# Kernel optimization log

Hardware: AMD Instinct MI355X
Metric: run time of the kernel (lower is better)

## Reference

```python
import jax, jax.numpy as jnp
import numpy as np

R, S, V, F = 4096, 128, 3, 35  # n_rays, n_samples, n_views(=3 fixed by rgb_fc), in_feat_ch+3


def _kaiming(key, fan_out, fan_in):
    return jax.random.normal(key, (fan_out, fan_in), jnp.float32) * jnp.sqrt(2.0 / fan_in)


def setup_inputs() -> dict:
    key = jax.random.key(0)
    ks = jax.random.split(key, 8)
    rgb_feat = jax.random.normal(ks[0], (R, S, V, F), jnp.float32)
    # base_fc: 105 -> 64 -> 32
    bw1, bw2 = _kaiming(ks[1], 64, 105), _kaiming(ks[2], 32, 64)
    # vis_fc: 32 -> 32 -> 32
    vw1, vw2 = _kaiming(ks[3], 32, 32), _kaiming(ks[4], 32, 32)
    # rgb_fc: 96 -> 32 -> 16 -> 3
    rw1, rw2, rw3 = _kaiming(ks[5], 32, 96), _kaiming(ks[6], 16, 32), _kaiming(ks[7], 3, 16)
    z = jnp.zeros
    return {
        "rgb_feat": rgb_feat,
        "bw1": bw1, "bb1": z((64,)), "bw2": bw2, "bb2": z((32,)),
        "vw1": vw1, "vb1": z((32,)), "vw2": vw2, "vb2": z((32,)),
        "rw1": rw1, "rb1": z((32,)), "rw2": rw2, "rb2": z((16,)), "rw3": rw3, "rb3": z((3,)),
    }


def _lin(x, w, b):
    return x @ w.T + b


def reference(rgb_feat, bw1, bb1, bw2, bb2, vw1, vb1, vw2, vb2,
              rw1, rb1, rw2, rb2, rw3, rb3):
    elu = jax.nn.elu
    num_views = rgb_feat.shape[2]
    rgb_in = rgb_feat[..., :3]
    # fused mean/variance over the views axis (dim=2)
    mean = jnp.mean(rgb_feat, axis=2, keepdims=True)          # [R,S,1,F]
    var = jnp.mean((rgb_feat - mean) ** 2, axis=2, keepdims=True)
    globalfeat = jnp.concatenate([mean, var], axis=-1)         # [R,S,1,2F]
    x = jnp.concatenate(
        [jnp.broadcast_to(globalfeat, (rgb_feat.shape[0], rgb_feat.shape[1], num_views, globalfeat.shape[-1])),
         rgb_feat], axis=-1)                                   # [R,S,V,3F]
    x = elu(_lin(elu(_lin(x, bw1, bb1)), bw2, bb2))            # [R,S,V,32]
    x_vis = elu(_lin(elu(_lin(x / num_views, vw1, vb1)), vw2, vb2))
    x = x + x_vis
    h = x.reshape(x.shape[0], x.shape[1], num_views * 32)      # [R,S,96]
    rgb_out = jax.nn.sigmoid(_lin(elu(_lin(elu(_lin(h, rw1, rb1)), rw2, rb2)), rw3, rb3))
    return (rgb_in, rgb_out)
```

## Files before the change

### kernel.cpp

```cpp
#include <hip/hip_runtime.h>
#include <hip/hip_bf16.h>

#define NPTS      524288
#define OUT2_BASE 4718592
#define NBLK64    8192

using bf16x8 = __attribute__((ext_vector_type(8))) short;
using f32x4  = __attribute__((ext_vector_type(4))) float;

#define MFMA(a, b, c) __builtin_amdgcn_mfma_f32_16x16x32_bf16(a, b, c, 0, 0, 0)


__device__ __forceinline__ ushort f2bf(float f) {
    union { float f; unsigned u; } v; v.f = f;
    unsigned u = v.u;
    unsigned r = u + 0x7fffu + ((u >> 16) & 1u);
    return (ushort)(r >> 16);
}
__device__ __forceinline__ uint pack2(float a, float b) {
    union { __hip_bfloat162 h; uint u; } cv;
    cv.h = __float22bfloat162_rn(make_float2(a, b));
    return cv.u;
}
__device__ __forceinline__ float eluf(float x) {
    return fmaxf(x, 0.f) + __expf(fminf(x, 0.f)) - 1.f;
}
__device__ __forceinline__ float sigm(float x) { return 1.f / (1.f + __expf(-x)); }

__device__ __forceinline__ void load8(const float* __restrict__ p, float* d) {
    __builtin_memcpy(d, p, 16);
    __builtin_memcpy(d + 4, p + 4, 16);
}
__device__ __forceinline__ bf16x8 pk8(const float* x) {
    union { uint4 u; bf16x8 h; } cv;
    cv.u = make_uint4(pack2(x[0], x[1]), pack2(x[2], x[3]),
                      pack2(x[4], x[5]), pack2(x[6], x[7]));
    return cv.h;
}
__device__ __forceinline__ bf16x8 pk4u(uint a, uint b, uint c, uint d) {
    union { uint4 u; bf16x8 h; } cv;
    cv.u = make_uint4(a, b, c, d);
    return cv.h;
}
__device__ __forceinline__ bf16x8 ldw(const ushort* p) { return *(const bf16x8*)p; }

__global__ void prep_k(const float* __restrict__ bw1, const float* __restrict__ bw2,
                       const float* __restrict__ vw1, const float* __restrict__ vw2,
                       const float* __restrict__ rw1, const float* __restrict__ rw2,
                       ushort* __restrict__ w)
{
    int i = blockIdx.x * 256 + threadIdx.x;
    if (i < 6144) {
        int n = i / 96, k = i % 96;
        float val = 0.f;
        if (k < 35)                 val = bw1[n * 105 + k];
        else if (k >= 40 && k < 75) val = bw1[n * 105 + 35 + (k - 40)];
        w[i] = f2bf(val);
    } else if (i < 10752) {
        int t = i - 6144, n = t / 72, k = t % 72;
        w[i] = f2bf(k < 35 ? bw1[n * 105 + 70 + k] : 0.f);
    } else if (i < 13056) {
        int t = i - 10752, n = t / 72, k = t % 72;
        w[i] = f2bf(k < 64 ? bw2[n * 64 + k] : 0.f);
    } else if (i < 14336) {
        int t = i - 13056, n = t / 40, k = t % 40;
        w[i] = f2bf(k < 32 ? vw1[n * 32 + k] * (1.f / 3.f) : 0.f);
    } else if (i < 15616) {
        int t = i - 14336, n = t / 40, k = t % 40;
        w[i] = f2bf(k < 32 ? vw2[n * 32 + k] : 0.f);
    } else if (i < 18944) {
        int t = i - 15616, n = t / 104, k = t % 104;
        w[i] = f2bf(k < 96 ? rw1[n * 96 + k] : 0.f);
    } else if (i < 19584) {
        int t = i - 18944, n = t / 40, k = t % 40;
        w[i] = f2bf(k < 32 ? rw2[n * 32 + k] : 0.f);
    }
}

__global__ __launch_bounds__(256, 4) void mlp_k(
    const float* __restrict__ feat, const ushort* __restrict__ w,
    const float* __restrict__ bb1, const float* __restrict__ bb2,
    const float* __restrict__ vb1, const float* __restrict__ vb2,
    const float* __restrict__ rb1, const float* __restrict__ rb2,
    const float* __restrict__ rw3, const float* __restrict__ rb3,
    float* __restrict__ out)
{
    __shared__ __align__(16) ushort sh[4][4608];

    const int tid  = threadIdx.x;
    const int wave = tid >> 6;
    const int lane = tid & 63;
    const int n16  = lane & 15;
    const int quad = lane >> 4;
    char* const RA = (char*)sh[wave];
    char* const RB = (char*)sh[wave] + 6144;
    const int sw7 = n16 & 7;
    const int sw3 = n16 & 3;

    const long long pbase = (long long)blockIdx.x * 64 + wave * 16;
    const long long pt    = pbase + n16;
    const float* row = feat + pt * 105;

    const ushort* WG = w;
    const ushort* WF = w + 6144;
    const ushort* W2 = w + 10752;
    const ushort* V1 = w + 13056;
    const ushort* V2 = w + 14336;
    const ushort* R1 = w + 15616;
    const ushort* R2 = w + 18944;

    {
        float* o1 = out + pbase * 9;
        const float* f0 = feat + pbase * 105;
#pragma unroll
        for (int t = 0; t < 3; ++t) {
            int i = lane + t * 64;
            if (t < 2 || lane < 16) {
                int p = i / 9, r = i - p * 9, v = r / 3, c = r - v * 3;
                o1[i] = f0[p * 105 + v * 35 + c];
            }
        }
    }

    float A0[8], A1[8], A2[8];
    load8(row + 8 * quad,      A0);
    load8(row + 35 + 8 * quad, A1);
    load8(row + 70 + 8 * quad, A2);
    float E0[8] = {0,0,0,0,0,0,0,0}, E1[8] = {0,0,0,0,0,0,0,0}, E2[8] = {0,0,0,0,0,0,0,0};
    if (quad == 0) {
        load8(row + 32, E0);
        load8(row + 67, E1);
        if (pt == (long long)NPTS - 1) {
            E2[0] = row[102]; E2[1] = row[103]; E2[2] = row[104];
        } else {
            load8(row + 102, E2);
        }
    }
    float M[8], Vv[8], M4[8], V4[8];
#pragma unroll
    for (int j = 0; j < 8; ++j) {
        float a = A0[j], b = A1[j], c = A2[j];
        float m = (a + b + c) * (1.f / 3.f);
        float da = a - m, db = b - m, dc = c - m;
        M[j] = m; Vv[j] = (da * da + db * db + dc * dc) * (1.f / 3.f);
        float a4 = E0[j], b4 = E1[j], c4 = E2[j];
        float m4 = (a4 + b4 + c4) * (1.f / 3.f);
        float e4 = a4 - m4, f4 = b4 - m4, g4 = c4 - m4;
        M4[j] = m4; V4[j] = (e4 * e4 + f4 * f4 + g4 * g4) * (1.f / 3.f);
    }
    uint vPK[4], v4PK[4], m4PK[4];
#pragma unroll
    for (int i = 0; i < 4; ++i) {
        vPK[i]  = pack2(Vv[2 * i], Vv[2 * i + 1]);
        v4PK[i] = pack2(V4[2 * i], V4[2 * i + 1]);
        m4PK[i] = pack2(M4[2 * i], M4[2 * i + 1]);
    }
    bf16x8 XAv[3], XBv[3];
    XAv[0] = pk8(A0); XAv[1] = pk8(A1); XAv[2] = pk8(A2);
    const bf16x8 ZF = pk4u(0u, 0u, 0u, 0u);
    XBv[0] = ZF; XBv[1] = ZF; XBv[2] = ZF;
    if (quad == 0) { XBv[0] = pk8(E0); XBv[1] = pk8(E1); XBv[2] = pk8(E2); }
    const bf16x8 G0 = pk8(M);
    const int prevAddr = ((lane + 48) & 63) * 4;
    uint G1u[4], G2u[4];
#pragma unroll
    for (int i = 0; i < 4; ++i) {
        uint bv  = (uint)__builtin_amdgcn_ds_bpermute(prevAddr, (int)vPK[i]);
        uint bv4 = (uint)__builtin_amdgcn_ds_bpermute(prevAddr, (int)v4PK[i]);
        G1u[i] = (quad == 0) ? m4PK[i] : bv;
        G2u[i] = (quad == 0) ? bv : ((quad == 1) ? bv4 : 0u);
    }
    const bf16x8 G1 = pk4u(G1u[0], G1u[1], G1u[2], G1u[3]);
    const bf16x8 G2 = pk4u(G2u[0], G2u[1], G2u[2], G2u[3]);

    const f32x4 Z = {0.f, 0.f, 0.f, 0.f};

#pragma unroll
    for (int ntl = 0; ntl < 4; ++ntl) {
        const ushort* WGb = WG + (ntl * 16 + n16) * 96 + quad * 8;
        f32x4 Cg = MFMA(ldw(WGb), G0, Z);
        Cg = MFMA(ldw(WGb + 32), G1, Cg);
        Cg = MFMA(ldw(WGb + 64), G2, Cg);
        const ushort* WFb = WF + (ntl * 16 + n16) * 72 + quad * 8;
        const bf16x8 wf0 = ldw(WFb), wf1 = ldw(WFb + 32);
        const float4 bq = *(const float4*)(bb1 + ntl * 16 + quad * 4);
#pragma unroll
        for (int v = 0; v < 3; ++v) {
            f32x4 C = MFMA(wf0, XAv[v], Cg);
            C = MFMA(wf1, XBv[v], C);
            float e0 = eluf(C[0] + bq.x), e1 = eluf(C[1] + bq.y);
            float e2 = eluf(C[2] + bq.z), e3 = eluf(C[3] + bq.w);
            uint2 u; u.x = pack2(e0, e1); u.y = pack2(e2, e3);
            int slot = (ntl * 2 + (quad >> 1)) ^ sw7;
            *(uint2*)(RA + v * 2048 + n16 * 128 + slot * 16 + (quad & 1) * 8) = u;
        }
    }

    float h2r[3][2][4];
#pragma unroll
    for (int v = 0; v < 3; ++v) {
        const bf16x8 ha = *(const bf16x8*)(RA + v * 2048 + n16 * 128 + ((0 + quad) ^ sw7) * 16);
        const bf16x8 hb = *(const bf16x8*)(RA + v * 2048 + n16 * 128 + ((4 + quad) ^ sw7) * 16);
#pragma unroll
        for (int n2 = 0; n2 < 2; ++n2) {
            const ushort* W2b = W2 + (n2 * 16 + n16) * 72 + quad * 8;
            f32x4 C = MFMA(ldw(W2b), ha, Z);
            C = MFMA(ldw(W2b + 32), hb, C);
            const float4 bq = *(const float4*)(bb2 + n2 * 16 + quad * 4);
            float e0 = eluf(C[0] + bq.x), e1 = eluf(C[1] + bq.y);
            float e2 = eluf(C[2] + bq.z), e3 = eluf(C[3] + bq.w);
            h2r[v][n2][0] = e0; h2r[v][n2][1] = e1;
            h2r[v][n2][2] = e2; h2r[v][n2][3] = e3;
            uint2 u; u.x = pack2(e0, e1); u.y = pack2(e2, e3);
            int slot = (n2 * 2 + (quad >> 1)) ^ sw3;
            *(uint2*)(RB + v * 1024 + n16 * 64 + slot * 16 + (quad & 1) * 8) = u;
        }
    }

#pragma unroll
    for (int v = 0; v < 3; ++v) {
        const bf16x8 hf = *(const bf16x8*)(RB + v * 1024 + n16 * 64 + ((quad ^ sw3) * 16));
#pragma unroll
        for (int n2 = 0; n2 < 2; ++n2) {
            f32x4 C = MFMA(ldw(V1 + (n2 * 16 + n16) * 40 + quad * 8), hf, Z);
            const float4 bq = *(const float4*)(vb1 + n2 * 16 + quad * 4);
            float e0 = eluf(C[0] + bq.x), e1 = eluf(C[1] + bq.y);
            float e2 = eluf(C[2] + bq.z), e3 = eluf(C[3] + bq.w);
            uint2 u; u.x = pack2(e0, e1); u.y = pack2(e2, e3);
            int slot = (n2 * 2 + (quad >> 1)) ^ sw3;
            *(uint2*)(RA + v * 1024 + n16 * 64 + slot * 16 + (quad & 1) * 8) = u;
        }
    }

#pragma unroll
    for (int v = 0; v < 3; ++v) {
        const bf16x8 tf = *(const bf16x8*)(RA + v * 1024 + n16 * 64 + ((quad ^ sw3) * 16));
#pragma unroll
        for (int n2 = 0; n2 < 2; ++n2) {
            f32x4 C = MFMA(ldw(V2 + (n2 * 16 + n16) * 40 + quad * 8), tf, Z);
            const float4 bq = *(const float4*)(vb2 + n2 * 16 + quad * 4);
            float x0 = h2r[v][n2][0] + eluf(C[0] + bq.x);
            float x1 = h2r[v][n2][1] + eluf(C[1] + bq.y);
            float x2v = h2r[v][n2][2] + eluf(C[2] + bq.z);
            float x3 = h2r[v][n2][3] + eluf(C[3] + bq.w);
            uint2 u; u.x = pack2(x0, x1); u.y = pack2(x2v, x3);
            int slot = (4 * v + 2 * n2 + (quad >> 1)) ^ sw3;
            *(uint2*)(RB + n16 * 192 + slot * 16 + (quad & 1) * 8) = u;
        }
    }

    f32x4 CR[2] = {Z, Z};
#pragma unroll
    for (int v = 0; v < 3; ++v) {
        const bf16x8 xf = *(const bf16x8*)(RB + n16 * 192 + (((4 * v + quad) ^ sw3) * 16));
#pragma unroll
        for (int n2 = 0; n2 < 2; ++n2)
            CR[n2] = MFMA(ldw(R1 + (n2 * 16 + n16) * 104 + v * 32 + quad * 8), xf, CR[n2]);
    }
#pragma unroll
    for (int n2 = 0; n2 < 2; ++n2) {
        const float4 bq = *(const float4*)(rb1 + n2 * 16 + quad * 4);
        float e0 = eluf(CR[n2][0] + bq.x), e1 = eluf(CR[n2][1] + bq.y);
        float e2 = eluf(CR[n2][2] + bq.z), e3 = eluf(CR[n2][3] + bq.w);
        uint2 u; u.x = pack2(e0, e1); u.y = pack2(e2, e3);
        int slot = (n2 * 2 + (quad >> 1)) ^ sw3;
        *(uint2*)(RA + n16 * 64 + slot * 16 + (quad & 1) * 8) = u;
    }

    const bf16x8 rf = *(const bf16x8*)(RA + n16 * 64 + ((quad ^ sw3) * 16));
    f32x4 C3 = MFMA(ldw(R2 + n16 * 40 + quad * 8), rf, Z);
    const float4 bq2 = *(const float4*)(rb2 + quad * 4);
    float r0 = eluf(C3[0] + bq2.x), r1v = eluf(C3[1] + bq2.y);
    float r2v = eluf(C3[2] + bq2.z), r3 = eluf(C3[3] + bq2.w);

    const float4 w30 = *(const float4*)(rw3 + 0 * 16 + quad * 4);
    const float4 w31 = *(const float4*)(rw3 + 1 * 16 + quad * 4);
    const float4 w32 = *(const float4*)(rw3 + 2 * 16 + quad * 4);
    float s0 = r0 * w30.x + r1v * w30.y + r2v * w30.z + r3 * w30.w;
    float s1 = r0 * w31.x + r1v * w31.y + r2v * w31.z + r3 * w31.w;
    float s2 = r0 * w32.x + r1v * w32.y + r2v * w32.z + r3 * w32.w;
    s0 += __shfl_xor(s0, 16); s0 += __shfl_xor(s0, 32);
    s1 += __shfl_xor(s1, 16); s1 += __shfl_xor(s1, 32);
    s2 += __shfl_xor(s2, 16); s2 += __shfl_xor(s2, 32);
    if (quad == 0) {
        float* o2 = out + OUT2_BASE + pt * 3;
        o2[0] = sigm(s0 + rb3[0]);
        o2[1] = sigm(s1 + rb3[1]);
        o2[2] = sigm(s2 + rb3[2]);
    }
}

extern "C" void kernel_launch(void* const* d_in, const int* in_sizes, int n_in,
                              void* d_out, int out_size, void* d_ws, size_t ws_size,
                              hipStream_t stream) {
    const float* feat = (const float*)d_in[0];
    const float* bw1  = (const float*)d_in[1];
    const float* bb1  = (const float*)d_in[2];
    const float* bw2  = (const float*)d_in[3];
    const float* bb2  = (const float*)d_in[4];
    const float* vw1  = (const float*)d_in[5];
    const float* vb1  = (const float*)d_in[6];
    const float* vw2  = (const float*)d_in[7];
    const float* vb2  = (const float*)d_in[8];
    const float* rw1  = (const float*)d_in[9];
    const float* rb1  = (const float*)d_in[10];
    const float* rw2  = (const float*)d_in[11];
    const float* rb2  = (const float*)d_in[12];
    const float* rw3  = (const float*)d_in[13];
    const float* rb3  = (const float*)d_in[14];
    ushort* w  = (ushort*)d_ws;
    float* out = (float*)d_out;

    hipLaunchKernelGGL(prep_k, dim3(77), dim3(256), 0, stream,
                       bw1, bw2, vw1, vw2, rw1, rw2, w);
    hipLaunchKernelGGL(mlp_k, dim3(NBLK64), dim3(256), 0, stream,
                       feat, w, bb1, bb2, vb1, vb2, rb1, rb2, rw3, rb3, out);
}
```

Baseline: 433.9 us.

## Process views sequentially through whole MLP chain to shrink LDS and raise occupancy

Reorders the kernel so that each view runs the full base/vis/rgb_fc1 chain before the next view starts. The per-wave LDS scratch can then shrink from about 9 KB to 3.3 KB, and launch bounds rise from 4 to 8 blocks per CU. The final 16->3 layer moves from shuffle reductions to an LDS-staged per-lane dot product with coalesced stores. The cost is a longer serial dependency chain per view and tighter register limits, which could cause spills.

```diff
diff --git a/kernel.cpp b/kernel.cpp
--- a/kernel.cpp
+++ b/kernel.cpp
@@ -77,7 +77,7 @@
     }
 }
 
-__global__ __launch_bounds__(256, 4) void mlp_k(
+__global__ __launch_bounds__(256, 8) void mlp_k(
     const float* __restrict__ feat, const ushort* __restrict__ w,
     const float* __restrict__ bb1, const float* __restrict__ bb2,
     const float* __restrict__ vb1, const float* __restrict__ vb2,
@@ -85,15 +85,15 @@
     const float* __restrict__ rw3, const float* __restrict__ rb3,
     float* __restrict__ out)
 {
-    __shared__ __align__(16) ushort sh[4][4608];
+    __shared__ __align__(16) char sh[4][3328];
 
     const int tid  = threadIdx.x;
     const int wave = tid >> 6;
     const int lane = tid & 63;
     const int n16  = lane & 15;
     const int quad = lane >> 4;
-    char* const RA = (char*)sh[wave];
-    char* const RB = (char*)sh[wave] + 6144;
+    char* const B1 = sh[wave];
+    char* const B2 = sh[wave] + 2048;
     const int sw7 = n16 & 7;
     const int sw3 = n16 & 3;
 
@@ -175,32 +175,33 @@
 
     const f32x4 Z = {0.f, 0.f, 0.f, 0.f};
 
+    f32x4 Cg[4];
 #pragma unroll
     for (int ntl = 0; ntl < 4; ++ntl) {
         const ushort* WGb = WG + (ntl * 16 + n16) * 96 + quad * 8;
-        f32x4 Cg = MFMA(ldw(WGb), G0, Z);
-        Cg = MFMA(ldw(WGb + 32), G1, Cg);
-        Cg = MFMA(ldw(WGb + 64), G2, Cg);
-        const ushort* WFb = WF + (ntl * 16 + n16) * 72 + quad * 8;
-        const bf16x8 wf0 = ldw(WFb), wf1 = ldw(WFb + 32);
-        const float4 bq = *(const float4*)(bb1 + ntl * 16 + quad * 4);
-#pragma unroll
-        for (int v = 0; v < 3; ++v) {
-            f32x4 C = MFMA(wf0, XAv[v], Cg);
-            C = MFMA(wf1, XBv[v], C);
+        f32x4 c = MFMA(ldw(WGb), G0, Z);
+        c = MFMA(ldw(WGb + 32), G1, c);
+        Cg[ntl] = MFMA(ldw(WGb + 64), G2, c);
+    }
+
+    f32x4 CR[2] = {Z, Z};
+#pragma unroll
+    for (int v = 0; v < 3; ++v) {
+#pragma unroll
+        for (int ntl = 0; ntl < 4; ++ntl) {
+            const ushort* WFb = WF + (ntl * 16 + n16) * 72 + quad * 8;
+            f32x4 C = MFMA(ldw(WFb), XAv[v], Cg[ntl]);
+            C = MFMA(ldw(WFb + 32), XBv[v], C);
+            const float4 bq = *(const float4*)(bb1 + ntl * 16 + quad * 4);
             float e0 = eluf(C[0] + bq.x), e1 = eluf(C[1] + bq.y);
             float e2 = eluf(C[2] + bq.z), e3 = eluf(C[3] + bq.w);
             uint2 u; u.x = pack2(e0, e1); u.y = pack2(e2, e3);
             int slot = (ntl * 2 + (quad >> 1)) ^ sw7;
-            *(uint2*)(RA + v * 2048 + n16 * 128 + slot * 16 + (quad & 1) * 8) = u;
-        }
-    }
-
-    float h2r[3][2][4];
-#pragma unroll
-    for (int v = 0; v < 3; ++v) {
-        const bf16x8 ha = *(const bf16x8*)(RA + v * 2048 + n16 * 128 + ((0 + quad) ^ sw7) * 16);
-        const bf16x8 hb = *(const bf16x8*)(RA + v * 2048 + n16 * 128 + ((4 + quad) ^ sw7) * 16);
+            *(uint2*)(B1 + n16 * 128 + slot * 16 + (quad & 1) * 8) = u;
+        }
+        const bf16x8 ha = *(const bf16x8*)(B1 + n16 * 128 + ((quad ^ sw7) * 16));
+        const bf16x8 hb = *(const bf16x8*)(B1 + n16 * 128 + (((4 + quad) ^ sw7) * 16));
+        float h2r[2][4];
 #pragma unroll
         for (int n2 = 0; n2 < 2; ++n2) {
             const ushort* W2b = W2 + (n2 * 16 + n16) * 72 + quad * 8;
@@ -209,54 +210,47 @@
             const float4 bq = *(const float4*)(bb2 + n2 * 16 + quad * 4);
             float e0 = eluf(C[0] + bq.x), e1 = eluf(C[1] + bq.y);
             float e2 = eluf(C[2] + bq.z), e3 = eluf(C[3] + bq.w);
-            h2r[v][n2][0] = e0; h2r[v][n2][1] = e1;
-            h2r[v][n2][2] = e2; h2r[v][n2][3] = e3;
+            h2r[n2][0] = e0; h2r[n2][1] = e1; h2r[n2][2] = e2; h2r[n2][3] = e3;
             uint2 u; u.x = pack2(e0, e1); u.y = pack2(e2, e3);
             int slot = (n2 * 2 + (quad >> 1)) ^ sw3;
-            *(uint2*)(RB + v * 1024 + n16 * 64 + slot * 16 + (quad & 1) * 8) = u;
-        }
-    }
-
-#pragma unroll
-    for (int v = 0; v < 3; ++v) {
-        const bf16x8 hf = *(const bf16x8*)(RB + v * 1024 + n16 * 64 + ((quad ^ sw3) * 16));
-#pragma unroll
-        for (int n2 = 0; n2 < 2; ++n2) {
-            f32x4 C = MFMA(ldw(V1 + (n2 * 16 + n16) * 40 + quad * 8), hf, Z);
-            const float4 bq = *(const float4*)(vb1 + n2 * 16 + quad * 4);
-            float e0 = eluf(C[0] + bq.x), e1 = eluf(C[1] + bq.y);
-            float e2 = eluf(C[2] + bq.z), e3 = eluf(C[3] + bq.w);
-            uint2 u; u.x = pack2(e0, e1); u.y = pack2(e2, e3);
-            int slot = (n2 * 2 + (quad >> 1)) ^ sw3;
-            *(uint2*)(RA + v * 1024 + n16 * 64 + slot * 16 + (quad & 1) * 8) = u;
-        }
-    }
-
-#pragma unroll
-    for (int v = 0; v < 3; ++v) {
-        const bf16x8 tf = *(const bf16x8*)(RA + v * 1024 + n16 * 64 + ((quad ^ sw3) * 16));
-#pragma unroll
-        for (int n2 = 0; n2 < 2; ++n2) {
-            f32x4 C = MFMA(ldw(V2 + (n2 * 16 + n16) * 40 + quad * 8), tf, Z);
-            const float4 bq = *(const float4*)(vb2 + n2 * 16 + quad * 4);
-            float x0 = h2r[v][n2][0] + eluf(C[0] + bq.x);
-            float x1 = h2r[v][n2][1] + eluf(C[1] + bq.y);
-            float x2v = h2r[v][n2][2] + eluf(C[2] + bq.z);
-            float x3 = h2r[v][n2][3] + eluf(C[3] + bq.w);
-            uint2 u; u.x = pack2(x0, x1); u.y = pack2(x2v, x3);
-            int slot = (4 * v + 2 * n2 + (quad >> 1)) ^ sw3;
-            *(uint2*)(RB + n16 * 192 + slot * 16 + (quad & 1) * 8) = u;
-        }
-    }
-
-    f32x4 CR[2] = {Z, Z};
-#pragma unroll
-    for (int v = 0; v < 3; ++v) {
-        const bf16x8 xf = *(const bf16x8*)(RB + n16 * 192 + (((4 * v + quad) ^ sw3) * 16));
-#pragma unroll
-        for (int n2 = 0; n2 < 2; ++n2)
-            CR[n2] = MFMA(ldw(R1 + (n2 * 16 + n16) * 104 + v * 32 + quad * 8), xf, CR[n2]);
-    }
+            *(uint2*)(B2 + n16 * 80 + slot * 16 + (quad & 1) * 8) = u;
+        }
+        {
+            const bf16x8 hf = *(const bf16x8*)(B2 + n16 * 80 + ((quad ^ sw3) * 16));
+#pragma unroll
+            for (int n2 = 0; n2 < 2; ++n2) {
+                f32x4 C = MFMA(ldw(V1 + (n2 * 16 + n16) * 40 + quad * 8), hf, Z);
+                const float4 bq = *(const float4*)(vb1 + n2 * 16 + quad * 4);
+                float e0 = eluf(C[0] + bq.x), e1 = eluf(C[1] + bq.y);
+                float e2 = eluf(C[2] + bq.z), e3 = eluf(C[3] + bq.w);
+                uint2 u; u.x = pack2(e0, e1); u.y = pack2(e2, e3);
+                int slot = (n2 * 2 + (quad >> 1)) ^ sw3;
+                *(uint2*)(B2 + n16 * 80 + slot * 16 + (quad & 1) * 8) = u;
+            }
+        }
+        {
+            const bf16x8 tf = *(const bf16x8*)(B2 + n16 * 80 + ((quad ^ sw3) * 16));
+#pragma unroll
+            for (int n2 = 0; n2 < 2; ++n2) {
+                f32x4 C = MFMA(ldw(V2 + (n2 * 16 + n16) * 40 + quad * 8), tf, Z);
+                const float4 bq = *(const float4*)(vb2 + n2 * 16 + quad * 4);
+                float x0 = h2r[n2][0] + eluf(C[0] + bq.x);
+                float x1 = h2r[n2][1] + eluf(C[1] + bq.y);
+                float x2v = h2r[n2][2] + eluf(C[2] + bq.z);
+                float x3 = h2r[n2][3] + eluf(C[3] + bq.w);
+                uint2 u; u.x = pack2(x0, x1); u.y = pack2(x2v, x3);
+                int slot = (n2 * 2 + (quad >> 1)) ^ sw3;
+                *(uint2*)(B1 + n16 * 80 + slot * 16 + (quad & 1) * 8) = u;
+            }
+        }
+        {
+            const bf16x8 xf = *(const bf16x8*)(B1 + n16 * 80 + ((quad ^ sw3) * 16));
+#pragma unroll
+            for (int n2 = 0; n2 < 2; ++n2)
+                CR[n2] = MFMA(ldw(R1 + (n2 * 16 + n16) * 104 + v * 32 + quad * 8), xf, CR[n2]);
+        }
+    }
+
 #pragma unroll
     for (int n2 = 0; n2 < 2; ++n2) {
         const float4 bq = *(const float4*)(rb1 + n2 * 16 + quad * 4);
@@ -264,29 +258,33 @@
         float e2 = eluf(CR[n2][2] + bq.z), e3 = eluf(CR[n2][3] + bq.w);
         uint2 u; u.x = pack2(e0, e1); u.y = pack2(e2, e3);
         int slot = (n2 * 2 + (quad >> 1)) ^ sw3;
-        *(uint2*)(RA + n16 * 64 + slot * 16 + (quad & 1) * 8) = u;
-    }
-
-    const bf16x8 rf = *(const bf16x8*)(RA + n16 * 64 + ((quad ^ sw3) * 16));
-    f32x4 C3 = MFMA(ldw(R2 + n16 * 40 + quad * 8), rf, Z);
-    const float4 bq2 = *(const float4*)(rb2 + quad * 4);
-    float r0 = eluf(C3[0] + bq2.x), r1v = eluf(C3[1] + bq2.y);
-    float r2v = eluf(C3[2] + bq2.z), r3 = eluf(C3[3] + bq2.w);
-
-    const float4 w30 = *(const float4*)(rw3 + 0 * 16 + quad * 4);
-    const float4 w31 = *(const float4*)(rw3 + 1 * 16 + quad * 4);
-    const float4 w32 = *(const float4*)(rw3 + 2 * 16 + quad * 4);
-    float s0 = r0 * w30.x + r1v * w30.y + r2v * w30.z + r3 * w30.w;
-    float s1 = r0 * w31.x + r1v * w31.y + r2v * w31.z + r3 * w31.w;
-    float s2 = r0 * w32.x + r1v * w32.y + r2v * w32.z + r3 * w32.w;
-    s0 += __shfl_xor(s0, 16); s0 += __shfl_xor(s0, 32);
-    s1 += __shfl_xor(s1, 16); s1 += __shfl_xor(s1, 32);
-    s2 += __shfl_xor(s2, 16); s2 += __shfl_xor(s2, 32);
-    if (quad == 0) {
-        float* o2 = out + OUT2_BASE + pt * 3;
-        o2[0] = sigm(s0 + rb3[0]);
-        o2[1] = sigm(s1 + rb3[1]);
-        o2[2] = sigm(s2 + rb3[2]);
+        *(uint2*)(B2 + n16 * 80 + slot * 16 + (quad & 1) * 8) = u;
+    }
+
+    {
+        const bf16x8 rf = *(const bf16x8*)(B2 + n16 * 80 + ((quad ^ sw3) * 16));
+        f32x4 C3 = MFMA(ldw(R2 + n16 * 40 + quad * 8), rf, Z);
+        const float4 bq2 = *(const float4*)(rb2 + quad * 4);
+        float4 rv;
+        rv.x = eluf(C3[0] + bq2.x);
+        rv.y = eluf(C3[1] + bq2.y);
+        rv.z = eluf(C3[2] + bq2.z);
+        rv.w = eluf(C3[3] + bq2.w);
+        *(float4*)(B1 + n16 * 80 + quad * 16) = rv;
+    }
+
+    if (lane < 48) {
+        int p = lane / 3, c = lane - p * 3;
+        const float4* rr = (const float4*)(B1 + p * 80);
+        const float4* w3 = (const float4*)(rw3 + c * 16);
+        float4 a0 = rr[0], a1 = rr[1], a2 = rr[2], a3 = rr[3];
+        float4 q0 = w3[0], q1 = w3[1], q2 = w3[2], q3 = w3[3];
+        float s = rb3[c];
+        s += a0.x * q0.x + a0.y * q0.y + a0.z * q0.z + a0.w * q0.w;
+        s += a1.x * q1.x + a1.y * q1.y + a1.z * q1.z + a1.w * q1.w;
+        s += a2.x * q2.x + a2.y * q2.y + a2.z * q2.z + a2.w * q2.w;
+        s += a3.x * q3.x + a3.y * q3.y + a3.z * q3.z + a3.w * q3.w;
+        out[OUT2_BASE + pbase * 3 + lane] = sigm(s);
     }
 }
 
```

Measured after the change: 1.149 ms. +164.8%, slower.
